# Optimization experiments

Measured on AMD Instinct MI355X. Metric: run time of the kernel, lower is better.

The kernel has to match this reference:

```python
import jax, jax.numpy as jnp
import numpy as np

ALPHA = 1.0
BETA = 0.5

B, N, E = 4096, 4096, 16384


def setup_inputs() -> dict:
    key = jax.random.key(0)
    k1, k2, k3, k4, k5 = jax.random.split(key, 5)
    outputs = jax.random.normal(k1, (B, N), dtype=jnp.float32)
    targets = jax.random.uniform(k2, (B, N), dtype=jnp.float32)
    # per-node level weight (equivalent to node_levels dict -> level_weights lookup)
    level_w = jax.random.uniform(k3, (N,), dtype=jnp.float32)
    edge_src = jax.random.randint(k4, (E,), 0, N, dtype=jnp.int32)  # parent i
    edge_dst = jax.random.randint(k5, (E,), 0, N, dtype=jnp.int32)  # child  j
    return {"outputs": outputs, "targets": targets, "level_w": level_w,
            "edge_src": edge_src, "edge_dst": edge_dst}


def reference(outputs, targets, level_w, edge_src, edge_dst):
    # BCEWithLogits, reduction='none': softplus(x) - x*t (numerically stable)
    bce = jax.nn.softplus(outputs) - outputs * targets          # [B, N]
    weighted_bce = bce * level_w[None, :]                        # [B, N]

    probs = jax.nn.sigmoid(outputs)                              # [B, N]
    # for each edge (i=parent, j=child): consistency[:, j] += relu(p[:, j] - p[:, i])
    diff = jax.nn.relu(probs[:, edge_dst] - probs[:, edge_src])  # [B, E]
    consistency = jnp.zeros_like(probs).at[:, edge_dst].add(diff)  # [B, N]

    return ALPHA * weighted_bce.mean() + BETA * consistency.mean()
```

## Files before the change

### kernel.cpp

```cpp
#include <hip/hip_runtime.h>
#include <math.h>


#define ALPHA_C 1.0f
#define BETA_C  0.5f

constexpr int B = 4096;
constexpr int N = 4096;
constexpr int E = 16384;
constexpr int THREADS = 1024;
constexpr int R = 4;

__global__ __launch_bounds__(64) void init_out_kernel(float* out) {
    if (threadIdx.x == 0) out[0] = 0.0f;
}

__device__ __forceinline__ void fast_sig_sp(float x, float& p, float& sp) {
    float q = __expf(-fabsf(x));
    float d = 1.0f + q;
    float r = __builtin_amdgcn_rcpf(d);
    p  = (x >= 0.0f) ? r : q * r;
    sp = fmaxf(x, 0.0f) + __logf(d);
}

__device__ __forceinline__ float edge4(const float4* __restrict__ p, int s, int d) {
    float4 a = p[s];
    float4 c = p[d];
    return fmaxf(c.x - a.x, 0.0f) + fmaxf(c.y - a.y, 0.0f) +
           fmaxf(c.z - a.z, 0.0f) + fmaxf(c.w - a.w, 0.0f);
}

__global__ __launch_bounds__(THREADS) void hier_loss_kernel(
    const float* __restrict__ outputs,
    const float* __restrict__ targets,
    const float* __restrict__ level_w,
    const int*   __restrict__ edge_src,
    const int*   __restrict__ edge_dst,
    float*       __restrict__ out)
{
    __shared__ float4 p_lds[N];

    const int r0  = blockIdx.x * R;
    const int tid = threadIdx.x;

    float s1 = 0.0f;
#pragma unroll
    for (int j = 0; j < N / THREADS; ++j) {
        const int n = tid + j * THREADS;
        const float w = level_w[n];
        float pv[R];
#pragma unroll
        for (int r = 0; r < R; ++r) {
            const float x = outputs[(size_t)(r0 + r) * N + n];
            const float t = targets[(size_t)(r0 + r) * N + n];
            float p, sp;
            fast_sig_sp(x, p, sp);
            s1 = fmaf(w, sp - x * t, s1);
            pv[r] = p;
        }
        p_lds[n] = make_float4(pv[0], pv[1], pv[2], pv[3]);
    }
    __syncthreads();

    float s2a = 0.0f, s2b = 0.0f;
    const int4* es4 = (const int4*)edge_src;
    const int4* ed4 = (const int4*)edge_dst;
#pragma unroll
    for (int j = 0; j < E / 4 / THREADS; ++j) {
        const int i = tid + j * THREADS;
        const int4 s = es4[i];
        const int4 d = ed4[i];
        s2a += edge4(p_lds, s.x, d.x);
        s2b += edge4(p_lds, s.y, d.y);
        s2a += edge4(p_lds, s.z, d.z);
        s2b += edge4(p_lds, s.w, d.w);
    }
    float s2 = s2a + s2b;

#pragma unroll
    for (int off = 32; off > 0; off >>= 1) {
        s1 += __shfl_down(s1, off, 64);
        s2 += __shfl_down(s2, off, 64);
    }
    __syncthreads();
    float* red = (float*)p_lds;
    const int wave = tid >> 6;
    const int lane = tid & 63;
    if (lane == 0) { red[wave] = s1; red[16 + wave] = s2; }
    __syncthreads();
    if (tid == 0) {
        float a = 0.0f, c = 0.0f;
#pragma unroll
        for (int w = 0; w < 16; ++w) { a += red[w]; c += red[16 + w]; }
        const float inv = 1.0f / ((float)B * (float)N);
        atomicAdd(out, (ALPHA_C * a + BETA_C * c) * inv);
    }
}

extern "C" void kernel_launch(void* const* d_in, const int* in_sizes, int n_in,
                              void* d_out, int out_size, void* d_ws, size_t ws_size,
                              hipStream_t stream) {
    const float* outputs = (const float*)d_in[0];
    const float* targets = (const float*)d_in[1];
    const float* level_w = (const float*)d_in[2];
    const int*   edge_src = (const int*)d_in[3];
    const int*   edge_dst = (const int*)d_in[4];
    float* out = (float*)d_out;

    init_out_kernel<<<1, 64, 0, stream>>>(out);
    hier_loss_kernel<<<B / R, THREADS, 0, stream>>>(outputs, targets, level_w,
                                                    edge_src, edge_dst, out);
}
```

Measured before the change: 157.9 us.

## Store probabilities as fp16x8 in LDS and process 8 rows per block

Stores sigmoid probabilities in shared memory as packed half-precision vectors of 8 rows instead of fp32 float4 of 4 rows. This doubles the rows handled per block and halves the number of blocks. Each edge gather now serves twice as many rows, and the edge loop's relu-difference uses packed fp16 math. Global loads of outputs, targets and weights are vectorised to float4. The consistency term loses precision because probabilities and per-thread accumulators are fp16, and the halved block count lowers parallelism.

```diff
diff --git a/kernel.cpp b/kernel.cpp
--- a/kernel.cpp
+++ b/kernel.cpp
@@ -9,7 +9,9 @@
 constexpr int N = 4096;
 constexpr int E = 16384;
 constexpr int THREADS = 1024;
-constexpr int R = 4;
+constexpr int R = 8;
+
+typedef _Float16 h8 __attribute__((ext_vector_type(8)));
 
 __global__ __launch_bounds__(64) void init_out_kernel(float* out) {
     if (threadIdx.x == 0) out[0] = 0.0f;
@@ -23,14 +25,7 @@
     sp = fmaxf(x, 0.0f) + __logf(d);
 }
 
-__device__ __forceinline__ float edge4(const float4* __restrict__ p, int s, int d) {
-    float4 a = p[s];
-    float4 c = p[d];
-    return fmaxf(c.x - a.x, 0.0f) + fmaxf(c.y - a.y, 0.0f) +
-           fmaxf(c.z - a.z, 0.0f) + fmaxf(c.w - a.w, 0.0f);
-}
-
-__global__ __launch_bounds__(THREADS) void hier_loss_kernel(
+__global__ __launch_bounds__(THREADS, 8) void hier_loss_kernel(
     const float* __restrict__ outputs,
     const float* __restrict__ targets,
     const float* __restrict__ level_w,
@@ -38,31 +33,43 @@
     const int*   __restrict__ edge_dst,
     float*       __restrict__ out)
 {
-    __shared__ float4 p_lds[N];
+    __shared__ h8 P[N];
 
     const int r0  = blockIdx.x * R;
     const int tid = threadIdx.x;
 
+    const float4* out4 = (const float4*)outputs;
+    const float4* tgt4 = (const float4*)targets;
+    const float4* lw4  = (const float4*)level_w;
+
     float s1 = 0.0f;
-#pragma unroll
-    for (int j = 0; j < N / THREADS; ++j) {
-        const int n = tid + j * THREADS;
-        const float w = level_w[n];
-        float pv[R];
+    {
+        const float4 w = lw4[tid];
+        const float wv[4] = {w.x, w.y, w.z, w.w};
+        h8 tmp[4];
 #pragma unroll
         for (int r = 0; r < R; ++r) {
-            const float x = outputs[(size_t)(r0 + r) * N + n];
-            const float t = targets[(size_t)(r0 + r) * N + n];
-            float p, sp;
-            fast_sig_sp(x, p, sp);
-            s1 = fmaf(w, sp - x * t, s1);
-            pv[r] = p;
+            const int row = r0 + r;
+            const float4 x = out4[(size_t)row * (N / 4) + tid];
+            const float4 t = tgt4[(size_t)row * (N / 4) + tid];
+            const float xs[4] = {x.x, x.y, x.z, x.w};
+            const float ts[4] = {t.x, t.y, t.z, t.w};
+#pragma unroll
+            for (int k = 0; k < 4; ++k) {
+                float p, sp;
+                fast_sig_sp(xs[k], p, sp);
+                s1 = fmaf(wv[k], sp - xs[k] * ts[k], s1);
+                tmp[k][r] = (_Float16)p;
+            }
         }
-        p_lds[n] = make_float4(pv[0], pv[1], pv[2], pv[3]);
+#pragma unroll
+        for (int k = 0; k < 4; ++k) P[4 * tid + k] = tmp[k];
     }
     __syncthreads();
 
-    float s2a = 0.0f, s2b = 0.0f;
+    h8 acc0 = {0, 0, 0, 0, 0, 0, 0, 0};
+    h8 acc1 = {0, 0, 0, 0, 0, 0, 0, 0};
+    const h8 zero = {0, 0, 0, 0, 0, 0, 0, 0};
     const int4* es4 = (const int4*)edge_src;
     const int4* ed4 = (const int4*)edge_dst;
 #pragma unroll
@@ -70,12 +77,18 @@
         const int i = tid + j * THREADS;
         const int4 s = es4[i];
         const int4 d = ed4[i];
-        s2a += edge4(p_lds, s.x, d.x);
-        s2b += edge4(p_lds, s.y, d.y);
-        s2a += edge4(p_lds, s.z, d.z);
-        s2b += edge4(p_lds, s.w, d.w);
+        h8 a0 = P[s.x], c0 = P[d.x];
+        h8 a1 = P[s.y], c1 = P[d.y];
+        h8 a2 = P[s.z], c2 = P[d.z];
+        h8 a3 = P[s.w], c3 = P[d.w];
+        acc0 += __builtin_elementwise_max(c0 - a0, zero);
+        acc1 += __builtin_elementwise_max(c1 - a1, zero);
+        acc0 += __builtin_elementwise_max(c2 - a2, zero);
+        acc1 += __builtin_elementwise_max(c3 - a3, zero);
     }
-    float s2 = s2a + s2b;
+    float s2 = 0.0f;
+#pragma unroll
+    for (int l = 0; l < 8; ++l) s2 += (float)acc0[l] + (float)acc1[l];
 
 #pragma unroll
     for (int off = 32; off > 0; off >>= 1) {
@@ -83,7 +96,7 @@
         s2 += __shfl_down(s2, off, 64);
     }
     __syncthreads();
-    float* red = (float*)p_lds;
+    float* red = (float*)P;
     const int wave = tid >> 6;
     const int lane = tid & 63;
     if (lane == 0) { red[wave] = s1; red[16 + wave] = s2; }
```

New measurement: 159.6 us. Within noise of the previous version (+1.1%).
